# Kernel optimization log

Hardware: AMD Instinct MI355X
Metric: run time of the kernel (lower is better)

The kernel has to match this reference:

```python
import jax, jax.numpy as jnp
import numpy as np

B, L, D = 2, 2048, 2048
H, KV = 32, 8
HD = D // H          # 64
REP = H // KV        # 4


def setup_inputs() -> dict:
    key = jax.random.key(0)
    ks = jax.random.split(key, 6)
    x = jax.random.normal(ks[0], (B, L, D), dtype=jnp.float32)
    # weights stored [in, out] (transpose of torch Linear weight), scaled for stability
    wq = jax.random.normal(ks[1], (D, H * HD), dtype=jnp.float32) * 0.02
    wk = jax.random.normal(ks[2], (D, KV * HD), dtype=jnp.float32) * 0.02
    wv = jax.random.normal(ks[3], (D, KV * HD), dtype=jnp.float32) * 0.02
    wo = jax.random.normal(ks[4], (H * HD, D), dtype=jnp.float32) * 0.02
    # RoPE frequencies: freqs_cis = exp(i * pos * theta), theta_j = 10000^{-2j/HD}
    inv_freq = 1.0 / (10000.0 ** (jnp.arange(0, HD, 2, dtype=jnp.float32) / HD))  # [HD/2]
    angles = jnp.arange(L, dtype=jnp.float32)[:, None] * inv_freq[None, :]        # [L, HD/2]
    freqs_cos = jnp.cos(angles)
    freqs_sin = jnp.sin(angles)
    # additive causal mask [L, L] (prefill from start_pos=0)
    mask = jnp.where(jnp.tril(jnp.ones((L, L), dtype=bool)), 0.0, -jnp.inf).astype(jnp.float32)
    return {"x": x, "start_pos": 0, "freqs_cos": freqs_cos, "freqs_sin": freqs_sin,
            "mask": mask, "wq": wq, "wk": wk, "wv": wv, "wo": wo}


def _apply_rope(t, cos, sin):
    # t: [B, L, h, HD]; cos/sin: [L, HD/2] -> broadcast [1, L, 1, HD/2]
    tp = t.reshape(*t.shape[:-1], HD // 2, 2)
    a, b = tp[..., 0], tp[..., 1]
    c = cos[None, :, None, :]
    s = sin[None, :, None, :]
    ra = a * c - b * s
    rb = a * s + b * c
    return jnp.stack([ra, rb], axis=-1).reshape(t.shape)


def reference(x, start_pos, freqs_cos, freqs_sin, mask, wq, wk, wv, wo):
    xq = jnp.einsum('bld,de->ble', x, wq).reshape(B, L, H, HD)
    xk = jnp.einsum('bld,de->ble', x, wk).reshape(B, L, KV, HD)
    xv = jnp.einsum('bld,de->ble', x, wv).reshape(B, L, KV, HD)
    xq = _apply_rope(xq, freqs_cos, freqs_sin)
    xk = _apply_rope(xk, freqs_cos, freqs_sin)
    # (cache write of xk/xv is a dead side effect in the torch module; omitted)
    # GQA: query head (g*REP + r) attends to kv head g  == repeat_interleave semantics
    q = xq.transpose(0, 2, 1, 3).reshape(B, KV, REP, L, HD)  # [B,KV,REP,L,HD]
    k = xk.transpose(0, 2, 1, 3)                              # [B,KV,L,HD]
    v = xv.transpose(0, 2, 1, 3)
    scale = 1.0 / jnp.sqrt(jnp.float32(HD))
    scores = jnp.einsum('bgrld,bgmd->bgrlm', q, k) * scale + mask  # [B,KV,REP,L,L]
    attn = jax.nn.softmax(scores, axis=-1)
    out = jnp.einsum('bgrlm,bgmd->bgrld', attn, v)            # [B,KV,REP,L,HD]
    out = out.reshape(B, H, L, HD).transpose(0, 2, 1, 3).reshape(B, L, H * HD)
    return jnp.einsum('ble,ed->bld', out, wo)
```

## Files before the change

### kernel.cpp

```cpp
#include <hip/hip_runtime.h>
#include <hip/hip_bf16.h>
#include <math.h>

typedef __bf16 bf16_t;
typedef __bf16 bf16x8 __attribute__((ext_vector_type(8)));
typedef __bf16 bf16x4 __attribute__((ext_vector_type(4)));
typedef __bf16 bf16x2 __attribute__((ext_vector_type(2)));
typedef float  f32x4  __attribute__((ext_vector_type(4)));
typedef int    i32x4  __attribute__((ext_vector_type(4)));

#define B_  2
#define L_  2048
#define D_  2048
#define H_  32
#define KV_ 8
#define HD_ 64

static __device__ __forceinline__ void gload_lds16(const bf16_t* g, void* l)
{
    __builtin_amdgcn_global_load_lds(
        (const __attribute__((address_space(1))) void*)g,
        (__attribute__((address_space(3))) void*)l, 16, 0, 0);
}

static __device__ __forceinline__ int packbf(float a, float b)
{
    bf16x2 t; t[0] = (bf16_t)a; t[1] = (bf16_t)b;
    return __builtin_bit_cast(int, t);
}

static __device__ __forceinline__ void pl32(int& a, int& b)
{
    asm("v_permlane32_swap_b32 %0, %1" : "+v"(a), "+v"(b));
}
static __device__ __forceinline__ void pl16(int& a, int& b)
{
    asm("v_permlane16_swap_b32 %0, %1" : "+v"(a), "+v"(b));
}

#define WAITV8() asm volatile("s_waitcnt vmcnt(8)" ::: "memory")
#define WAITV0() asm volatile("s_waitcnt vmcnt(0)" ::: "memory")
#define WAITL0() asm volatile("s_waitcnt lgkmcnt(0)" ::: "memory")

__global__ void cast_f32_bf16(const float4* __restrict__ in,
                              bf16x4* __restrict__ out, int n4)
{
    const int i = blockIdx.x * 256 + threadIdx.x;
    if (i >= n4) return;
    const float4 v = in[i];
    bf16x4 o;
    o[0] = (bf16_t)v.x; o[1] = (bf16_t)v.y; o[2] = (bf16_t)v.z; o[3] = (bf16_t)v.w;
    out[i] = o;
}

template <typename InT>
__global__ void transpose_cast(const InT* __restrict__ in, bf16_t* __restrict__ out,
                               int R, int C)
{
    __shared__ bf16_t tile[32][33];
    const int bx = blockIdx.x * 32, by = blockIdx.y * 32;
    in  += (size_t)blockIdx.z * R * C;
    out += (size_t)blockIdx.z * R * C;
    const int tx = threadIdx.x, ty = threadIdx.y;
#pragma unroll
    for (int i = ty; i < 32; i += 8)
        tile[i][tx] = (bf16_t)(float)in[(size_t)(by + i) * C + bx + tx];
    __syncthreads();
#pragma unroll
    for (int i = ty; i < 32; i += 8)
        out[(size_t)(bx + i) * R + by + tx] = tile[tx][i];
}

template <typename OutT>
__global__ __launch_bounds__(256) void gemm_tn(
    const bf16_t* __restrict__ A,
    const bf16_t* __restrict__ BT,
    OutT* __restrict__ C,
    int M, int N, int K)
{
    __shared__ __attribute__((aligned(16))) bf16_t As[128 * 32];
    __shared__ __attribute__((aligned(16))) bf16_t Bs[128 * 32];

    const int m0   = blockIdx.y * 128;
    const int n0   = blockIdx.x * 128;
    const int tid  = threadIdx.x;
    const int wave = tid >> 6;
    const int lane = tid & 63;
    const int quad = lane >> 4;
    const int l16  = lane & 15;
    const int wm   = (wave & 1) * 64;
    const int wn   = (wave >> 1) * 64;
    const int sr   = tid >> 2;
    const int sc   = (tid & 3) * 8;

    f32x4 acc[4][4];
    const f32x4 zf = {0.f, 0.f, 0.f, 0.f};
#pragma unroll
    for (int i = 0; i < 4; i++)
#pragma unroll
        for (int j = 0; j < 4; j++) acc[i][j] = zf;

    const bf16_t* ag = A  + (size_t)(m0 + sr) * K + sc;
    const bf16_t* bg = BT + (size_t)(n0 + sr) * K + sc;
    bf16_t* asl = As + tid * 8;
    bf16_t* bsl = Bs + tid * 8;

    for (int k0 = 0; k0 < K; k0 += 32) {
        gload_lds16(ag + k0,                  asl);
        gload_lds16(ag + (size_t)64 * K + k0, asl + 2048);
        gload_lds16(bg + k0,                  bsl);
        gload_lds16(bg + (size_t)64 * K + k0, bsl + 2048);
        __syncthreads();

        bf16x8 af[4], bfr[4];
#pragma unroll
        for (int i = 0; i < 4; i++)
            af[i] = *(const bf16x8*)(&As[(wm + i * 16 + l16) * 32 + quad * 8]);
#pragma unroll
        for (int i = 0; i < 4; i++)
            bfr[i] = *(const bf16x8*)(&Bs[(wn + i * 16 + l16) * 32 + quad * 8]);

#pragma unroll
        for (int mi = 0; mi < 4; mi++)
#pragma unroll
            for (int ni = 0; ni < 4; ni++)
                acc[mi][ni] = __builtin_amdgcn_mfma_f32_16x16x32_bf16(
                    af[mi], bfr[ni], acc[mi][ni], 0, 0, 0);
        __syncthreads();
    }

#pragma unroll
    for (int mi = 0; mi < 4; mi++)
#pragma unroll
        for (int ni = 0; ni < 4; ni++)
#pragma unroll
            for (int r = 0; r < 4; r++) {
                const int row = m0 + wm + mi * 16 + quad * 4 + r;
                const int col = n0 + wn + ni * 16 + l16;
                C[(size_t)row * N + col] = (OutT)acc[mi][ni][r];
            }
}

__global__ __launch_bounds__(256) void gemm_qkv(
    const bf16_t* __restrict__ A,
    const bf16_t* __restrict__ BT,
    bf16_t* __restrict__ Qb, bf16_t* __restrict__ Kb, bf16_t* __restrict__ Vb,
    int K)
{
    __shared__ __attribute__((aligned(16))) bf16_t As[128 * 32];
    __shared__ __attribute__((aligned(16))) bf16_t Bs[128 * 32];

    const int m0   = blockIdx.y * 128;
    const int n0   = blockIdx.x * 128;
    const int tid  = threadIdx.x;
    const int wave = tid >> 6;
    const int lane = tid & 63;
    const int quad = lane >> 4;
    const int l16  = lane & 15;
    const int wm   = (wave & 1) * 64;
    const int wn   = (wave >> 1) * 64;
    const int sr   = tid >> 2;
    const int sc   = (tid & 3) * 8;

    f32x4 acc[4][4];
    const f32x4 zf = {0.f, 0.f, 0.f, 0.f};
#pragma unroll
    for (int i = 0; i < 4; i++)
#pragma unroll
        for (int j = 0; j < 4; j++) acc[i][j] = zf;

    const bf16_t* ag = A  + (size_t)(m0 + sr) * K + sc;
    const bf16_t* bg = BT + (size_t)(n0 + sr) * K + sc;
    bf16_t* asl = As + tid * 8;
    bf16_t* bsl = Bs + tid * 8;

    for (int k0 = 0; k0 < K; k0 += 32) {
        gload_lds16(ag + k0,                  asl);
        gload_lds16(ag + (size_t)64 * K + k0, asl + 2048);
        gload_lds16(bg + k0,                  bsl);
        gload_lds16(bg + (size_t)64 * K + k0, bsl + 2048);
        __syncthreads();

        bf16x8 af[4], bfr[4];
#pragma unroll
        for (int i = 0; i < 4; i++)
            af[i] = *(const bf16x8*)(&As[(wm + i * 16 + l16) * 32 + quad * 8]);
#pragma unroll
        for (int i = 0; i < 4; i++)
            bfr[i] = *(const bf16x8*)(&Bs[(wn + i * 16 + l16) * 32 + quad * 8]);

#pragma unroll
        for (int mi = 0; mi < 4; mi++)
#pragma unroll
            for (int ni = 0; ni < 4; ni++)
                acc[mi][ni] = __builtin_amdgcn_mfma_f32_16x16x32_bf16(
                    af[mi], bfr[ni], acc[mi][ni], 0, 0, 0);
        __syncthreads();
    }

    bf16_t* Cb; int ldc, coff; float cscale = 1.f;
    if (n0 < 2048)      { Cb = Qb; ldc = 2048; coff = 0; }
    else if (n0 < 2560) { Cb = Kb; ldc = 512;  coff = 2048;
                          cscale = 0.18033688011112042f; }
    else                { Cb = Vb; ldc = 512;  coff = 2560; }

#pragma unroll
    for (int mi = 0; mi < 4; mi++)
#pragma unroll
        for (int ni = 0; ni < 4; ni++)
#pragma unroll
            for (int r = 0; r < 4; r++) {
                const int row = m0 + wm + mi * 16 + quad * 4 + r;
                const int col = n0 + wn + ni * 16 + l16 - coff;
                Cb[(size_t)row * ldc + col] = (bf16_t)(acc[mi][ni][r] * cscale);
            }
}

__global__ void rope_k(bf16_t* __restrict__ T, const float* __restrict__ fc,
                       const float* __restrict__ fs, int nheads, int total8)
{
    const int idx = blockIdx.x * 256 + threadIdx.x;
    if (idx >= total8) return;
    const int g  = idx & 7;
    const int t  = idx >> 3;
    const int h  = t % nheads;
    const int bl = t / nheads;
    const int l  = bl & (L_ - 1);
    const float4 c4 = *(const float4*)(fc + l * 32 + g * 4);
    const float4 s4 = *(const float4*)(fs + l * 32 + g * 4);
    const size_t off = ((size_t)bl * nheads + h) * 64 + g * 8;
    const bf16x8 v = *(const bf16x8*)(T + off);
    const float cc[4] = {c4.x, c4.y, c4.z, c4.w};
    const float ss[4] = {s4.x, s4.y, s4.z, s4.w};
    bf16x8 o;
#pragma unroll
    for (int p = 0; p < 4; p++) {
        const float a  = (float)v[2 * p];
        const float b2 = (float)v[2 * p + 1];
        o[2 * p]     = (bf16_t)(a * cc[p] - b2 * ss[p]);
        o[2 * p + 1] = (bf16_t)(a * ss[p] + b2 * cc[p]);
    }
    *(bf16x8*)(T + off) = o;
}

__global__ __launch_bounds__(256, 2) void attn_k(
    const bf16_t* __restrict__ Q,
    const bf16_t* __restrict__ Kc,
    const bf16_t* __restrict__ VT,
    bf16_t* __restrict__ Ob)
{
    __shared__ __attribute__((aligned(16))) char LDS[65536];
    float* OL = (float*)LDS;
    float* LR = (float*)(LDS + 17408);

    const int tid  = threadIdx.x;
    const int wave = tid >> 6;
    const int lane = tid & 63;
    const int quad = lane >> 4;
    const int l16  = lane & 15;

    const int id   = blockIdx.y * 16 + blockIdx.x;
    const int c    = (id >> 3) & 15;
    const int bh   = (id & 7) * 8 + (id >> 7);
    const int bb   = bh >> 5;
    const int h    = bh & 31;
    const int kvh  = h >> 2;
    const size_t bbL = (size_t)bb * L_;

    const int schunk = ((lane & 3) ^ ((lane >> 3) & 3)) * 8;
    const int sw16   = ((l16 >> 1) & 3) * 16;

    const bf16_t* Kg = Kc + bbL * (KV_ * HD_) + kvh * HD_;
    const bf16_t* Vg = VT + (size_t)(bb * KV_ + kvh) * HD_ * L_;
    const bf16_t* KgL = Kg + (size_t)(wave * 32 + (lane >> 2)) * (KV_ * HD_) + schunk;
    const bf16_t* VgL = Vg + (size_t)(lane >> 2) * L_ + wave * 32 + schunk;
    char* kdst0 = (char*)LDS + wave * 2048 + (lane << 4);
    char* vdst0 = (char*)LDS + 16384 + wave * 4096 + (lane << 4);

    const f32x4 zf = {0.f, 0.f, 0.f, 0.f};

    for (int half = 0; half < 2; ++half) {
        const int j     = half ? c : 31 - c;
        const int qbase = j * 64;
        const int nkt   = (j + 2) >> 1;

        bf16x8 qf[4][2];
#pragma unroll
        for (int qt = 0; qt < 4; qt++) {
            const bf16_t* qrow = Q + ((bbL + qbase + qt * 16 + l16) * H_ + h) * HD_;
            qf[qt][0] = *(const bf16x8*)(qrow + quad * 8);
            qf[qt][1] = *(const bf16x8*)(qrow + 32 + quad * 8);
        }

        f32x4 acc[4][4];
#pragma unroll
        for (int mt = 0; mt < 4; mt++)
#pragma unroll
            for (int qt = 0; qt < 4; qt++) acc[mt][qt] = zf;
        float lacc[4] = {0.f, 0.f, 0.f, 0.f};

        {
            const int ktb = 0;
#pragma unroll
            for (int cc = 0; cc < 2; cc++)
#pragma unroll
                for (int sub = 0; sub < 2; sub++)
                    gload_lds16(KgL + (size_t)(ktb + sub * 16) * (KV_ * HD_) + cc * 32,
                                kdst0 + cc * 8192 + sub * 1024);
#pragma unroll
            for (int sub = 0; sub < 4; sub++)
                gload_lds16(VgL + (size_t)(sub * 16) * L_ + ktb,
                            vdst0 + sub * 1024);
        }

        for (int kt = 0; kt < nkt; kt++) {
            if (kt + 1 < nkt) {
                WAITL0();
                const int d = ((kt + 1) & 1) * 32768;
                const int ktb = (kt + 1) * 128;
#pragma unroll
                for (int cc = 0; cc < 2; cc++)
#pragma unroll
                    for (int sub = 0; sub < 2; sub++)
                        gload_lds16(KgL + (size_t)(ktb + sub * 16) * (KV_ * HD_) + cc * 32,
                                    kdst0 + d + cc * 8192 + sub * 1024);
#pragma unroll
                for (int sub = 0; sub < 4; sub++)
                    gload_lds16(VgL + (size_t)(sub * 16) * L_ + ktb,
                                vdst0 + d + sub * 1024);
                WAITV8();
            } else {
                WAITV0();
            }

            const char* Kld = LDS + (kt & 1) * 32768;
            const char* Vld = Kld + 16384;

            bf16x8 kf[2][2];
#pragma unroll
            for (int t = 0; t < 2; t++)
#pragma unroll
                for (int cc = 0; cc < 2; cc++)
                    kf[t][cc] = *(const bf16x8*)(Kld + cc * 8192 +
                        (wave * 32 + t * 16 + l16) * 64 + ((quad * 16) ^ sw16));

            bf16x8 vf[4];
#pragma unroll
            for (int mt = 0; mt < 4; mt++)
                vf[mt] = *(const bf16x8*)(Vld + wave * 4096 +
                    (mt * 16 + l16) * 64 + ((quad * 16) ^ sw16));

            f32x4 st[2][4];
            __builtin_amdgcn_s_setprio(1);
#pragma unroll
            for (int t = 0; t < 2; t++)
#pragma unroll
                for (int qt = 0; qt < 4; qt++) {
                    f32x4 s = __builtin_amdgcn_mfma_f32_16x16x32_bf16(
                        kf[t][0], qf[qt][0], zf, 0, 0, 0);
                    st[t][qt] = __builtin_amdgcn_mfma_f32_16x16x32_bf16(
                        kf[t][1], qf[qt][1], s, 0, 0, 0);
                }
            __builtin_amdgcn_s_setprio(0);

            if (kt == nkt - 1) {
                const int kq = kt * 128 + wave * 32 + quad * 4 - qbase - l16;
#pragma unroll
                for (int t = 0; t < 2; t++)
#pragma unroll
                    for (int qt = 0; qt < 4; qt++)
#pragma unroll
                        for (int r = 0; r < 4; r++)
                            st[t][qt][r] = (kq + t * 16 - qt * 16 + r <= 0)
                                         ? st[t][qt][r] : -__builtin_inff();
            }

            int pk[2][4][2];
#pragma unroll
            for (int t = 0; t < 2; t++)
#pragma unroll
                for (int qt = 0; qt < 4; qt++) {
                    const float e0 = __builtin_amdgcn_exp2f(st[t][qt][0]);
                    const float e1 = __builtin_amdgcn_exp2f(st[t][qt][1]);
                    const float e2 = __builtin_amdgcn_exp2f(st[t][qt][2]);
                    const float e3 = __builtin_amdgcn_exp2f(st[t][qt][3]);
                    lacc[qt] += (e0 + e1) + (e2 + e3);
                    pk[t][qt][0] = packbf(e0, e1);
                    pk[t][qt][1] = packbf(e2, e3);
                }

#pragma unroll
            for (int qt = 0; qt < 4; qt++) {
                int a0 = pk[0][qt][0], b0 = pk[1][qt][0];
                pl32(a0, b0); pl16(a0, b0);
                int a1 = pk[0][qt][1], b1 = pk[1][qt][1];
                pl32(a1, b1); pl16(a1, b1);
                i32x4 bi;
                bi[0] = a0; bi[1] = a1; bi[2] = b0; bi[3] = b1;
                const bf16x8 pb = __builtin_bit_cast(bf16x8, bi);
                __builtin_amdgcn_s_setprio(1);
#pragma unroll
                for (int mt = 0; mt < 4; mt++)
                    acc[mt][qt] = __builtin_amdgcn_mfma_f32_16x16x32_bf16(
                        vf[mt], pb, acc[mt][qt], 0, 0, 0);
                __builtin_amdgcn_s_setprio(0);
            }
        }

        float lw[4];
#pragma unroll
        for (int qt = 0; qt < 4; qt++) {
            float v = lacc[qt];
            v += __shfl_xor(v, 16);
            v += __shfl_xor(v, 32);
            lw[qt] = v;
        }

        __syncthreads();

        if (quad == 0)
#pragma unroll
            for (int qt = 0; qt < 4; qt++)
                LR[(wave * 4 + qt) * 16 + l16] = lw[qt];

#pragma unroll
        for (int p = 0; p < 4; p++) {
#pragma unroll
            for (int qt = 0; qt < 4; qt++) {
                if (((qt - wave) & 3) == p) {
#pragma unroll
                    for (int mt = 0; mt < 4; mt++) {
                        float* a = OL + (qt * 16 + l16) * 68 + mt * 16 + quad * 4;
                        if (p == 0) *(f32x4*)a = acc[mt][qt];
                        else        *(f32x4*)a = *(f32x4*)a + acc[mt][qt];
                    }
                }
            }
            __syncthreads();
        }

        const float ls = LR[(0 * 4 + wave) * 16 + l16] + LR[(1 * 4 + wave) * 16 + l16]
                       + LR[(2 * 4 + wave) * 16 + l16] + LR[(3 * 4 + wave) * 16 + l16];
        const float inv = 1.f / ls;
        bf16_t* orow = Ob + ((bbL + qbase + wave * 16 + l16) * H_ + h) * HD_;
#pragma unroll
        for (int j2 = 0; j2 < 4; j2++) {
            const f32x4 v = *(const f32x4*)(OL + (wave * 16 + l16) * 68 + quad * 16 + j2 * 4);
            bf16x4 o;
#pragma unroll
            for (int i = 0; i < 4; i++) o[i] = (bf16_t)(v[i] * inv);
            *(bf16x4*)(orow + quad * 16 + j2 * 4) = o;
        }
        __syncthreads();
    }
}

extern "C" void kernel_launch(void* const* d_in, const int* in_sizes, int n_in,
                              void* d_out, int out_size, void* d_ws, size_t ws_size,
                              hipStream_t stream)
{
    (void)in_sizes; (void)n_in; (void)out_size; (void)ws_size;
    const float* xf = (const float*)d_in[0];
    const float* fc = (const float*)d_in[2];
    const float* fs = (const float*)d_in[3];
    const float* wq = (const float*)d_in[5];
    const float* wk = (const float*)d_in[6];
    const float* wv = (const float*)d_in[7];
    const float* wo = (const float*)d_in[8];
    float* out = (float*)d_out;

    char* ws = (char*)d_ws;
    bf16_t* xb   = (bf16_t*)(ws);
    bf16_t* Qb   = (bf16_t*)(ws + (16ull << 20));
    bf16_t* Kb   = (bf16_t*)(ws + (32ull << 20));
    bf16_t* Vb   = (bf16_t*)(ws + (36ull << 20));
    bf16_t* VTb  = (bf16_t*)(ws + (40ull << 20));
    bf16_t* Oa   = (bf16_t*)(ws + (44ull << 20));
    bf16_t* Wqkv = (bf16_t*)(ws + (60ull << 20));
    bf16_t* WoT  = (bf16_t*)(ws + (72ull << 20));

    cast_f32_bf16<<<8192, 256, 0, stream>>>((const float4*)xf, (bf16x4*)xb,
                                            B_ * L_ * D_ / 4);

    const dim3 tb(32, 8);
    transpose_cast<float><<<dim3(64, 64, 1), tb, 0, stream>>>(wq, Wqkv, 2048, 2048);
    transpose_cast<float><<<dim3(16, 64, 1), tb, 0, stream>>>(wk, Wqkv + 2048ull * 2048, 2048, 512);
    transpose_cast<float><<<dim3(16, 64, 1), tb, 0, stream>>>(wv, Wqkv + 2560ull * 2048, 2048, 512);
    transpose_cast<float><<<dim3(64, 64, 1), tb, 0, stream>>>(wo, WoT, 2048, 2048);

    gemm_qkv<<<dim3(24, 32), 256, 0, stream>>>(xb, Wqkv, Qb, Kb, Vb, 2048);

    rope_k<<<4096, 256, 0, stream>>>(Qb, fc, fs, 32, B_ * L_ * 32 * 8);
    rope_k<<<1024, 256, 0, stream>>>(Kb, fc, fs, 8, B_ * L_ * 8 * 8);

    transpose_cast<bf16_t><<<dim3(16, 64, 2), tb, 0, stream>>>(Vb, VTb, 2048, 512);

    attn_k<<<dim3(16, 64), 256, 0, stream>>>(Qb, Kb, VTb, Oa);

    gemm_tn<float><<<dim3(16, 32), 256, 0, stream>>>(Oa, WoT, out, 4096, 2048, 2048);
}
```

Before: 349.2 us.

## Rewrite QKV GEMM with 256x256 tiles, double-buffered swizzled LDS and phased MFMA

```diff
diff --git a/kernel.cpp b/kernel.cpp
--- a/kernel.cpp
+++ b/kernel.cpp
@@ -39,6 +39,7 @@
 }
 
 #define WAITV8() asm volatile("s_waitcnt vmcnt(8)" ::: "memory")
+#define WAITV4() asm volatile("s_waitcnt vmcnt(4)" ::: "memory")
 #define WAITV0() asm volatile("s_waitcnt vmcnt(0)" ::: "memory")
 #define WAITL0() asm volatile("s_waitcnt lgkmcnt(0)" ::: "memory")
 
@@ -141,80 +142,178 @@
             }
 }
 
-__global__ __launch_bounds__(256) void gemm_qkv(
+#define FRAG(base, row, kk) \
+    (*(const bf16x8*)((base) + (size_t)(row) * 128 + ((((kk) * 4 + quad) ^ sw8) << 4)))
+
+#define STG_A(kt, h, buf) do {                                                        \
+    gload_lds16(Ag + (size_t)((h) * 128)      * 2048 + (size_t)(kt) * 64,             \
+                sdst + (buf) * 32768 + (h) * 16384);                                  \
+    gload_lds16(Ag + (size_t)((h) * 128 + 64) * 2048 + (size_t)(kt) * 64,             \
+                sdst + (buf) * 32768 + (h) * 16384 + 8192);                           \
+} while (0)
+
+#define STG_B(kt, h, buf) do {                                                        \
+    gload_lds16(Bg + (size_t)((h) * 128)      * 2048 + (size_t)(kt) * 64,             \
+                sdst + 65536 + (buf) * 32768 + (h) * 16384);                          \
+    gload_lds16(Bg + (size_t)((h) * 128 + 64) * 2048 + (size_t)(kt) * 64,             \
+                sdst + 65536 + (buf) * 32768 + (h) * 16384 + 8192);                   \
+} while (0)
+
+#define PHASE_SET(AB, BB, STG1, STG2, STG3, STG4, VM4)                                \
+  {                                        \
+    _Pragma("unroll") for (int m = 0; m < 4; m++) {                                   \
+        Afr[m][0] = FRAG(AB, arow + m * 16, 0);                                       \
+        Afr[m][1] = FRAG(AB, arow + m * 16, 1); }                                     \
+    _Pragma("unroll") for (int n = 0; n < 2; n++) {                                   \
+        B01[n][0] = FRAG(BB, brow + n * 16, 0);                                       \
+        B01[n][1] = FRAG(BB, brow + n * 16, 1); }                                     \
+    STG1;                                                                             \
+    asm volatile("s_waitcnt lgkmcnt(8)" ::: "memory");                                \
+    __builtin_amdgcn_s_barrier();                                                     \
+    WAITL0();                                                                         \
+    __builtin_amdgcn_s_setprio(1);                                                    \
+    _Pragma("unroll") for (int m = 0; m < 4; m++)                                     \
+      _Pragma("unroll") for (int n = 0; n < 2; n++)                                   \
+        _Pragma("unroll") for (int kk = 0; kk < 2; kk++)                              \
+          acc[m][n] = __builtin_amdgcn_mfma_f32_16x16x32_bf16(                        \
+              Afr[m][kk], B01[n][kk], acc[m][n], 0, 0, 0);                            \
+    __builtin_amdgcn_s_setprio(0);                                                    \
+    __builtin_amdgcn_s_barrier();                                                     \
+  }                                                                                   \
+  {                                                 \
+    _Pragma("unroll") for (int n = 0; n < 2; n++) {                                   \
+        B23[n][0] = FRAG(BB, brow + (n + 2) * 16, 0);                                 \
+        B23[n][1] = FRAG(BB, brow + (n + 2) * 16, 1); }                               \
+    STG2;                                                                             \
+    __builtin_amdgcn_s_barrier();                                                     \
+    WAITL0();                                                                         \
+    __builtin_amdgcn_s_setprio(1);                                                    \
+    _Pragma("unroll") for (int m = 0; m < 4; m++)                                     \
+      _Pragma("unroll") for (int n = 0; n < 2; n++)                                   \
+        _Pragma("unroll") for (int kk = 0; kk < 2; kk++)                              \
+          acc[m][n + 2] = __builtin_amdgcn_mfma_f32_16x16x32_bf16(                    \
+              Afr[m][kk], B23[n][kk], acc[m][n + 2], 0, 0, 0);                        \
+    __builtin_amdgcn_s_setprio(0);                                                    \
+    __builtin_amdgcn_s_barrier();                                                     \
+  }                                                                                   \
+  {                                                 \
+    _Pragma("unroll") for (int m = 0; m < 4; m++) {                                   \
+        Afr[m][0] = FRAG(AB, arow + (m + 4) * 16, 0);                                 \
+        Afr[m][1] = FRAG(AB, arow + (m + 4) * 16, 1); }                               \
+    STG3;                                                                             \
+    __builtin_amdgcn_s_barrier();                                                     \
+    WAITL0();                                                                         \
+    __builtin_amdgcn_s_setprio(1);                                                    \
+    _Pragma("unroll") for (int m = 0; m < 4; m++)                                     \
+      _Pragma("unroll") for (int n = 0; n < 2; n++)                                   \
+        _Pragma("unroll") for (int kk = 0; kk < 2; kk++)                              \
+          acc[m + 4][n + 2] = __builtin_amdgcn_mfma_f32_16x16x32_bf16(                \
+              Afr[m][kk], B23[n][kk], acc[m + 4][n + 2], 0, 0, 0);                    \
+    __builtin_amdgcn_s_setprio(0);                                                    \
+    __builtin_amdgcn_s_barrier();                                                     \
+  }                                                                                   \
+  {                                        \
+    STG4;                                                                             \
+    VM4;                                                                              \
+    __builtin_amdgcn_s_barrier();                                                     \
+    __builtin_amdgcn_s_setprio(1);                                                    \
+    _Pragma("unroll") for (int m = 0; m < 4; m++)                                     \
+      _Pragma("unroll") for (int n = 0; n < 2; n++)                                   \
+        _Pragma("unroll") for (int kk = 0; kk < 2; kk++)                              \
+          acc[m + 4][n] = __builtin_amdgcn_mfma_f32_16x16x32_bf16(                    \
+              Afr[m][kk], B01[n][kk], acc[m + 4][n], 0, 0, 0);                        \
+    __builtin_amdgcn_s_setprio(0);                                                    \
+    __builtin_amdgcn_s_barrier();                                                     \
+  }
+
+__global__ __launch_bounds__(512, 2) void gemm_qkv(
     const bf16_t* __restrict__ A,
     const bf16_t* __restrict__ BT,
-    bf16_t* __restrict__ Qb, bf16_t* __restrict__ Kb, bf16_t* __restrict__ Vb,
-    int K)
-{
-    __shared__ __attribute__((aligned(16))) bf16_t As[128 * 32];
-    __shared__ __attribute__((aligned(16))) bf16_t Bs[128 * 32];
-
-    const int m0   = blockIdx.y * 128;
-    const int n0   = blockIdx.x * 128;
+    bf16_t* __restrict__ Qb, bf16_t* __restrict__ Kb, bf16_t* __restrict__ Vb)
+{
+    extern __shared__ __attribute__((aligned(16))) char DLDS[];
+    constexpr int NITER = 2048 / 64 / 2;
+
     const int tid  = threadIdx.x;
     const int wave = tid >> 6;
     const int lane = tid & 63;
     const int quad = lane >> 4;
     const int l16  = lane & 15;
-    const int wm   = (wave & 1) * 64;
-    const int wn   = (wave >> 1) * 64;
-    const int sr   = tid >> 2;
-    const int sc   = (tid & 3) * 8;
-
-    f32x4 acc[4][4];
+    const int wr   = wave >> 2;
+    const int wc   = wave & 3;
+    const int m0   = blockIdx.y * 256;
+    const int n0   = blockIdx.x * 256;
+
+    const int srow  = tid >> 3;
+    const int swcol = ((tid & 7) ^ (srow & 7)) * 8;
+    const bf16_t* Ag = A  + (size_t)(m0 + srow) * 2048 + swcol;
+    const bf16_t* Bg = BT + (size_t)(n0 + srow) * 2048 + swcol;
+    char* sdst = DLDS + tid * 16;
+
+    const char* AB0 = DLDS;
+    const char* AB1 = DLDS + 32768;
+    const char* BB0 = DLDS + 65536;
+    const char* BB1 = DLDS + 98304;
+    const int sw8  = l16 & 7;
+    const int arow = wr * 128 + l16;
+    const int brow = wc * 64 + l16;
+
+    f32x4 acc[8][4];
     const f32x4 zf = {0.f, 0.f, 0.f, 0.f};
 #pragma unroll
-    for (int i = 0; i < 4; i++)
+    for (int i = 0; i < 8; i++)
 #pragma unroll
         for (int j = 0; j < 4; j++) acc[i][j] = zf;
 
-    const bf16_t* ag = A  + (size_t)(m0 + sr) * K + sc;
-    const bf16_t* bg = BT + (size_t)(n0 + sr) * K + sc;
-    bf16_t* asl = As + tid * 8;
-    bf16_t* bsl = Bs + tid * 8;
-
-    for (int k0 = 0; k0 < K; k0 += 32) {
-        gload_lds16(ag + k0,                  asl);
-        gload_lds16(ag + (size_t)64 * K + k0, asl + 2048);
-        gload_lds16(bg + k0,                  bsl);
-        gload_lds16(bg + (size_t)64 * K + k0, bsl + 2048);
-        __syncthreads();
-
-        bf16x8 af[4], bfr[4];
-#pragma unroll
-        for (int i = 0; i < 4; i++)
-            af[i] = *(const bf16x8*)(&As[(wm + i * 16 + l16) * 32 + quad * 8]);
-#pragma unroll
-        for (int i = 0; i < 4; i++)
-            bfr[i] = *(const bf16x8*)(&Bs[(wn + i * 16 + l16) * 32 + quad * 8]);
-
-#pragma unroll
-        for (int mi = 0; mi < 4; mi++)
-#pragma unroll
-            for (int ni = 0; ni < 4; ni++)
-                acc[mi][ni] = __builtin_amdgcn_mfma_f32_16x16x32_bf16(
-                    af[mi], bfr[ni], acc[mi][ni], 0, 0, 0);
-        __syncthreads();
+    bf16x8 Afr[4][2], B01[2][2], B23[2][2];
+
+    STG_B(0, 0, 0); STG_B(0, 1, 0); STG_A(0, 0, 0); STG_A(0, 1, 0);
+    STG_B(1, 0, 1); STG_B(1, 1, 1);
+    WAITV4();
+    __builtin_amdgcn_s_barrier();
+
+    for (int i = 0; i < NITER; ++i) {
+        const int t1 = 2 * i + 1;
+        const int t2 = 2 * i + 2;
+        const int t3 = 2 * i + 3;
+        const bool more = (i + 1 < NITER);
+
+        PHASE_SET(AB0, BB0,
+                  STG_A(t1, 0, 1),
+                  STG_A(t1, 1, 1),
+                  if (more) STG_B(t2, 0, 0),
+                  if (more) STG_B(t2, 1, 0),
+                  if (more) { WAITV4(); } else { WAITV0(); })
+        PHASE_SET(AB1, BB1,
+                  if (more) STG_A(t2, 0, 0),
+                  if (more) STG_A(t2, 1, 0),
+                  if (more) STG_B(t3, 0, 1),
+                  if (more) STG_B(t3, 1, 1),
+                  WAITV4())
     }
 
-    bf16_t* Cb; int ldc, coff; float cscale = 1.f;
+    bf16_t* Cb; int ldc, coff; float cs = 1.f;
     if (n0 < 2048)      { Cb = Qb; ldc = 2048; coff = 0; }
     else if (n0 < 2560) { Cb = Kb; ldc = 512;  coff = 2048;
-                          cscale = 0.18033688011112042f; }
+                          cs = 0.18033688011112042f; }
     else                { Cb = Vb; ldc = 512;  coff = 2560; }
 
 #pragma unroll
-    for (int mi = 0; mi < 4; mi++)
-#pragma unroll
-        for (int ni = 0; ni < 4; ni++)
+    for (int mt = 0; mt < 8; mt++)
+#pragma unroll
+        for (int nt = 0; nt < 4; nt++)
 #pragma unroll
             for (int r = 0; r < 4; r++) {
-                const int row = m0 + wm + mi * 16 + quad * 4 + r;
-                const int col = n0 + wn + ni * 16 + l16 - coff;
-                Cb[(size_t)row * ldc + col] = (bf16_t)(acc[mi][ni][r] * cscale);
+                const int row = m0 + wr * 128 + mt * 16 + quad * 4 + r;
+                const int col = n0 + wc * 64 + nt * 16 + l16 - coff;
+                Cb[(size_t)row * ldc + col] = (bf16_t)(acc[mt][nt][r] * cs);
             }
 }
+
+#undef FRAG
+#undef STG_A
+#undef STG_B
+#undef PHASE_SET
 
 __global__ void rope_k(bf16_t* __restrict__ T, const float* __restrict__ fc,
                        const float* __restrict__ fs, int nheads, int total8)
@@ -488,7 +587,7 @@
     transpose_cast<float><<<dim3(16, 64, 1), tb, 0, stream>>>(wv, Wqkv + 2560ull * 2048, 2048, 512);
     transpose_cast<float><<<dim3(64, 64, 1), tb, 0, stream>>>(wo, WoT, 2048, 2048);
 
-    gemm_qkv<<<dim3(24, 32), 256, 0, stream>>>(xb, Wqkv, Qb, Kb, Vb, 2048);
+    gemm_qkv<<<dim3(12, 16), 512, 131072, stream>>>(xb, Wqkv, Qb, Kb, Vb);
 
     rope_k<<<4096, 256, 0, stream>>>(Qb, fc, fs, 32, B_ * L_ * 32 * 8);
     rope_k<<<1024, 256, 0, stream>>>(Kb, fc, fs, 8, B_ * L_ * 8 * 8);
```

Measured after the change: 330.2 us. 1.06x faster.
